# Kernel optimization log

Hardware: AMD Instinct MI355X
Metric: run time of the kernel (lower is better)

Reference implementation:

```python
import jax, jax.numpy as jnp
import numpy as np

B, N, DIM = 4, 1024, 768
H, HD = 12, DIM // 12
GP = 49
MLP = 3072


def _layernorm(x, w, b, eps=1e-5):
    mu = x.mean(axis=-1, keepdims=True)
    var = ((x - mu) ** 2).mean(axis=-1, keepdims=True)
    return (x - mu) * jax.lax.rsqrt(var + eps) * w + b


def setup_inputs() -> dict:
    key = jax.random.key(0)
    ks = jax.random.split(key, 12)
    s = 0.02
    return {
        "x": jax.random.normal(ks[0], (B, N, DIM), jnp.float32),
        "ln1_w": jnp.ones((DIM,), jnp.float32),
        "ln1_b": jnp.zeros((DIM,), jnp.float32),
        "qkv_w": jax.random.normal(ks[1], (DIM, 3 * DIM), jnp.float32) * s,
        "qkv_b": jnp.zeros((3 * DIM,), jnp.float32),
        "proj_w": jax.random.normal(ks[2], (DIM, DIM), jnp.float32) * s,
        "proj_b": jnp.zeros((DIM,), jnp.float32),
        "gp_w": jax.random.normal(ks[3], (GP, DIM), jnp.float32) * s,  # nn.Linear(dim, gp_num).weight, shape (gp_num, dim)
        "alpha": jax.random.normal(ks[4], (1, H, 1, 1), jnp.float32),
        "ln2_w": jnp.ones((DIM,), jnp.float32),
        "ln2_b": jnp.zeros((DIM,), jnp.float32),
        "ff1_w": jax.random.normal(ks[5], (DIM, MLP), jnp.float32) * s,
        "ff1_b": jnp.zeros((MLP,), jnp.float32),
        "ff2_w": jax.random.normal(ks[6], (MLP, DIM), jnp.float32) * s,
        "ff2_b": jnp.zeros((DIM,), jnp.float32),
    }


def reference(x, ln1_w, ln1_b, qkv_w, qkv_b, proj_w, proj_b, gp_w, alpha,
              ln2_w, ln2_b, ff1_w, ff1_b, ff2_w, ff2_b):
    b, n, _ = x.shape
    # --- attention branch ---
    xn = _layernorm(x, ln1_w, ln1_b)
    qkv = xn @ qkv_w + qkv_b                                 # [b,n,3*dim]
    q, k, v = jnp.split(qkv, 3, axis=-1)
    to_heads = lambda t: t.reshape(b, n, H, HD).transpose(0, 2, 1, 3)  # [b,h,n,hd]
    q, k, v = to_heads(q), to_heads(k), to_heads(v)
    scale = HD ** -0.5
    attn = jnp.einsum('bhnd,bhmd->bhnm', q, k) * scale       # raw scores
    # group weights: view (gp_num, dim) -> (h, gp_num, hd) (row-major, same as torch .view)
    gp = gp_w.reshape(H, GP, HD)
    gw = jnp.einsum('bhnd,hmd->bhnm', v, gp)                 # [b,h,n,gp]
    gw = jax.nn.gelu(gw, approximate=False)
    gw = jax.nn.softmax(gw, axis=-1)
    gw = jnp.einsum('bhnm,bhkm->bhnk', gw, gw)               # [b,h,n,n]
    attn = jax.nn.softmax(attn * gw, axis=-1)
    a = jax.nn.sigmoid(alpha)
    attn = (1.0 - a) * attn + a * gw
    attn = attn / (attn.sum(axis=2, keepdims=True) + 1e-8)   # note: dim=2 (column renorm), faithful to source
    out = jnp.einsum('bhnm,bhmd->bhnd', attn, v)
    out = out.transpose(0, 2, 1, 3).reshape(b, n, DIM)
    out = out @ proj_w + proj_b
    x = out + x
    # --- FFN branch ---
    xn = _layernorm(x, ln2_w, ln2_b)
    hdn = jax.nn.gelu(xn @ ff1_w + ff1_b, approximate=False)
    x = (hdn @ ff2_w + ff2_b) + x
    return x
```

## Files before the change

### kernel.cpp

```cpp
#include <hip/hip_runtime.h>
#include <hip/hip_bf16.h>
#include <math.h>

#define DEVI __device__ __forceinline__

typedef __bf16 bf16x8 __attribute__((ext_vector_type(8)));
typedef float f32x4 __attribute__((ext_vector_type(4)));
typedef float f32x2 __attribute__((ext_vector_type(2)));
typedef unsigned int u32x4 __attribute__((ext_vector_type(4)));
typedef float f32x4v __attribute__((ext_vector_type(4)));
typedef unsigned short u16;
typedef unsigned char u8;

DEVI u16 f2bf(float f) {
    __hip_bfloat16 h = __float2bfloat16(f);
    return __builtin_bit_cast(u16, h);
}
DEVI float bf2f(u16 u) {
    unsigned int x = ((unsigned int)u) << 16;
    return __builtin_bit_cast(float, x);
}
DEVI float gelu_f(float x) {
    float y = 0.7978845608f * (x + 0.044715f * x * x * x);
    float e = __expf(2.f * y);
    float t = 1.f - 2.f / (e + 1.f);
    return 0.5f * x * (1.f + t);
}
DEVI float sigm(float x) { return 1.f / (1.f + __expf(-x)); }

DEVI bf16x8 ldfrag(const u16* p) {
    return __builtin_bit_cast(bf16x8, *reinterpret_cast<const u32x4*>(p));
}

DEVI void gload_lds16(const u16* g, u16* l) {
    __builtin_amdgcn_global_load_lds(
        (const __attribute__((address_space(1))) void*)g,
        (__attribute__((address_space(3))) void*)l, 16, 0, 0);
}

DEVI void stage8(const u16* gbase, long long stride, u16* lds, int lane) {
    int r = lane >> 3;
    int kg = (lane & 7) ^ r;
    gload_lds16(gbase + (long long)r * stride + kg * 8, lds);
}
DEVI bf16x8 fragsw(const u16* tile, int rr, int k) {
    return ldfrag(&tile[rr * 64 + ((k ^ (rr & 7)) << 3)]);
}

DEVI unsigned int packbf(float a, float b) {
    return __builtin_amdgcn_perm(__builtin_bit_cast(unsigned int, b),
                                 __builtin_bit_cast(unsigned int, a), 0x07060302u);
}

__global__ __launch_bounds__(256) void tcast_all(const float* __restrict__ qkv_w, const float* __restrict__ proj_w,
                                                 const float* __restrict__ ff1_w, const float* __restrict__ ff2_w,
                                                 const float* __restrict__ gp_w,
                                                 u16* __restrict__ wqkv, u16* __restrict__ wproj,
                                                 u16* __restrict__ wff1, u16* __restrict__ wff2,
                                                 u16* __restrict__ gpB) {
    int id = blockIdx.x;
    if (id >= 6912) {
        int h = id - 6912;
        int tid = threadIdx.y * 32 + threadIdx.x;
        for (int i = tid; i < 4096; i += 256) {
            int m = i >> 6, d = i & 63;
            float v = (m < 49) ? gp_w[h * 3136 + m * 64 + d] : 0.f;
            gpB[h * 4096 + i] = f2bf(v);
        }
        return;
    }
    const float* in; u16* out; int R, C, tx;
    if (id < 1728)      { in = qkv_w;  out = wqkv;  R = 768;  C = 2304; tx = 72; }
    else if (id < 2304) { in = proj_w; out = wproj; R = 768;  C = 768;  tx = 24; id -= 1728; }
    else if (id < 4608) { in = ff1_w;  out = wff1;  R = 768;  C = 3072; tx = 96; id -= 2304; }
    else                { in = ff2_w;  out = wff2;  R = 3072; C = 768;  tx = 24; id -= 4608; }
    int c0 = (id % tx) * 32, r0 = (id / tx) * 32;
    __shared__ float tile[32][33];
    for (int ry = threadIdx.y; ry < 32; ry += 8)
        tile[ry][threadIdx.x] = in[(long long)(r0 + ry) * C + c0 + threadIdx.x];
    __syncthreads();
    for (int cy = threadIdx.y; cy < 32; cy += 8)
        out[(long long)(c0 + cy) * R + r0 + threadIdx.x] = f2bf(tile[threadIdx.x][cy]);
}

__global__ __launch_bounds__(256) void ln_k(const float* __restrict__ parts, int nparts, long long pstride,
                                            const float* __restrict__ bias2, const float* __restrict__ in2,
                                            const float* __restrict__ w, const float* __restrict__ b,
                                            u16* __restrict__ outbf, float* __restrict__ x1out,
                                            float* __restrict__ zfill) {
    int row = blockIdx.x;
    if (zfill && row < 192) zfill[row * 256 + threadIdx.x] = 0.f;
    long long ro = (long long)row * 768;
    __shared__ float lds1[4], lds2[4];
    float v[3];
    float s = 0.f, sq = 0.f;
#pragma unroll
    for (int j = 0; j < 3; j++) {
        int c = threadIdx.x + j * 256;
        float x = 0.f;
        for (int p = 0; p < nparts; p++) x += parts[p * pstride + ro + c];
        if (bias2) x += bias2[c];
        if (in2) x += in2[ro + c];
        v[j] = x; s += x; sq += x * x;
    }
    if (x1out) {
#pragma unroll
        for (int j = 0; j < 3; j++) x1out[ro + threadIdx.x + j * 256] = v[j];
    }
    for (int off = 32; off; off >>= 1) { s += __shfl_down(s, off); sq += __shfl_down(sq, off); }
    int wid = threadIdx.x >> 6;
    if ((threadIdx.x & 63) == 0) { lds1[wid] = s; lds2[wid] = sq; }
    __syncthreads();
    s = lds1[0] + lds1[1] + lds1[2] + lds1[3];
    sq = lds2[0] + lds2[1] + lds2[2] + lds2[3];
    float mu = s * (1.f / 768.f);
    float var = sq * (1.f / 768.f) - mu * mu;
    float rs = rsqrtf(var + 1e-5f);
#pragma unroll
    for (int j = 0; j < 3; j++) {
        int c = threadIdx.x + j * 256;
        outbf[ro + c] = f2bf((v[j] - mu) * rs * w[c] + b[c]);
    }
}

struct GemmP {
    const u16* A; const u16* B;
    float* outF; u16* outB;
    const float* bias;
    u16* qh; u16* kh; u16* vh;
    int K, lda, ldb, ldc;
    long long pstride;
    int epi;
    int splits;
};

__global__ __launch_bounds__(256) void gemm_bt4(GemmP p) {
    __shared__ u16 As[128 * 64];
    __shared__ u16 Bs[128 * 64];
    const int tid = threadIdx.x, lane = tid & 63, wave = tid >> 6;
    const int l16 = lane & 15, qd = lane >> 4;
    const int bn0 = blockIdx.x * 128, bm0 = blockIdx.y * 128;
    const int wm0 = (wave >> 1) * 64, wn0 = (wave & 1) * 64;
    const int kc = p.K / p.splits;
    const int kbeg = blockIdx.z * kc, kend = kbeg + kc;
    f32x4 acc[4][4] = {};
    for (int k0 = kbeg; k0 < kend; k0 += 64) {
        __syncthreads();
#pragma unroll
        for (int t = 0; t < 4; t++) {
            int rowg = wave * 32 + t * 8;
            stage8(p.A + (long long)(bm0 + rowg) * p.lda + k0, p.lda, As + rowg * 64, lane);
            stage8(p.B + (long long)(bn0 + rowg) * p.ldb + k0, p.ldb, Bs + rowg * 64, lane);
        }
        __syncthreads();
#pragma unroll
        for (int s = 0; s < 2; s++) {
            bf16x8 af[4], bv[4];
#pragma unroll
            for (int i = 0; i < 4; i++) af[i] = fragsw(As, wm0 + i * 16 + l16, s * 4 + qd);
#pragma unroll
            for (int j = 0; j < 4; j++) bv[j] = fragsw(Bs, wn0 + j * 16 + l16, s * 4 + qd);
#pragma unroll
            for (int i = 0; i < 4; i++)
#pragma unroll
                for (int j = 0; j < 4; j++)
                    acc[i][j] = __builtin_amdgcn_mfma_f32_16x16x32_bf16(af[i], bv[j], acc[i][j], 0, 0, 0);
        }
    }
#pragma unroll
    for (int i = 0; i < 4; i++)
#pragma unroll
        for (int j = 0; j < 4; j++)
#pragma unroll
            for (int r = 0; r < 4; r++) {
                int row = bm0 + wm0 + i * 16 + qd * 4 + r;
                int col = bn0 + wn0 + j * 16 + l16;
                float v = acc[i][j][r];
                if (p.epi == 0) {
                    p.outF[(long long)blockIdx.z * p.pstride + (long long)row * p.ldc + col] = v;
                } else if (p.epi == 2) {
                    p.outB[(long long)row * p.ldc + col] = f2bf(gelu_f(v + p.bias[col]));
                } else {
                    v += p.bias[col];
                    int sect = col / 768, cc = col % 768;
                    int h = cc >> 6, d = cc & 63;
                    int b = row >> 10, n = row & 1023;
                    long long o = ((long long)(b * 12 + h) * 1024 + n) * 64 + d;
                    if (sect == 0) p.qh[o] = f2bf(v * 0.125f);
                    else if (sect == 1) p.kh[o] = f2bf(v);
                    else p.vh[o] = f2bf(v);
                }
            }
}

__global__ __launch_bounds__(256) void gw0m_k(const u16* __restrict__ vh, const u16* __restrict__ gpB,
                                              u16* __restrict__ gwn, float* __restrict__ Wt) {
    {
        long long zi = ((long long)blockIdx.y * 16 + blockIdx.x) * 256 + threadIdx.x;
        Wt[zi] = 0.f;
    }
    __shared__ u16 As[64 * 64];
    __shared__ u16 Bs[64 * 64];
    const int tid = threadIdx.x, lane = tid & 63, wave = tid >> 6;
    const int l16 = lane & 15, qd = lane >> 4;
    const int z = blockIdx.y, n0 = blockIdx.x * 64, h = z % 12;
    const u16* vz = vh + ((long long)z * 1024 + n0) * 64;
    const u16* gz = gpB + h * 4096;
#pragma unroll
    for (int t = 0; t < 2; t++) {
        int rowg = wave * 16 + t * 8;
        stage8(vz + (long long)rowg * 64, 64, As + rowg * 64, lane);
        stage8(gz + (long long)rowg * 64, 64, Bs + rowg * 64, lane);
    }
    __syncthreads();
    f32x4 acc[4] = {};
#pragma unroll
    for (int s = 0; s < 2; s++) {
        bf16x8 af = fragsw(As, wave * 16 + l16, s * 4 + qd);
#pragma unroll
        for (int j = 0; j < 4; j++) {
            bf16x8 bv = fragsw(Bs, j * 16 + l16, s * 4 + qd);
            acc[j] = __builtin_amdgcn_mfma_f32_16x16x32_bf16(af, bv, acc[j], 0, 0, 0);
        }
    }
    float ex[4][4];
#pragma unroll
    for (int r = 0; r < 4; r++) {
        float mx = -1e30f;
        float gv[4];
#pragma unroll
        for (int j = 0; j < 4; j++) {
            int col = j * 16 + l16;
            float g = gelu_f(acc[j][r]);
            gv[j] = g;
            if (col < 49) mx = fmaxf(mx, g);
            else gv[j] = -1e30f;
        }
        mx = fmaxf(mx, __shfl_xor(mx, 1)); mx = fmaxf(mx, __shfl_xor(mx, 2));
        mx = fmaxf(mx, __shfl_xor(mx, 4)); mx = fmaxf(mx, __shfl_xor(mx, 8));
        float s = 0.f;
#pragma unroll
        for (int j = 0; j < 4; j++) {
            int col = j * 16 + l16;
            float e = (col < 49) ? __expf(gv[j] - mx) : 0.f;
            ex[r][j] = e;
            s += e;
        }
        s += __shfl_xor(s, 1); s += __shfl_xor(s, 2);
        s += __shfl_xor(s, 4); s += __shfl_xor(s, 8);
        float inv = 1.f / s;
        int row = wave * 16 + qd * 4 + r;
        long long o = ((long long)z * 1024 + n0 + row) * 64;
#pragma unroll
        for (int j = 0; j < 4; j++)
            gwn[o + j * 16 + l16] = f2bf(ex[r][j] * inv);
    }
}

__global__ __launch_bounds__(256) void attn_tg4(const u16* __restrict__ qh, const u16* __restrict__ kh,
                                                const u16* __restrict__ gwn, u8* __restrict__ e8,
                                                float* __restrict__ rowsumE) {
    __shared__ u16 As[128 * 64];
    __shared__ u16 Bs[128 * 64];
    const int tid = threadIdx.x, lane = tid & 63, wave = tid >> 6;
    const int l16 = lane & 15, qd = lane >> 4;
    const int bn0 = blockIdx.x * 128, bm0 = blockIdx.y * 128, z = blockIdx.z;
    const int wm0 = (wave >> 1) * 64, wn0 = (wave & 1) * 64;
    const u16* qz = qh + (long long)z * 65536;
    const u16* kz = kh + (long long)z * 65536;
    const u16* gz = gwn + (long long)z * 65536;
    f32x4 accS[4][4] = {};
    f32x4 accG[4][4] = {};
#pragma unroll
    for (int t = 0; t < 4; t++) {
        int rowg = wave * 32 + t * 8;
        stage8(qz + (long long)(bm0 + rowg) * 64, 64, As + rowg * 64, lane);
        stage8(kz + (long long)(bn0 + rowg) * 64, 64, Bs + rowg * 64, lane);
    }
    __syncthreads();
#pragma unroll
    for (int s = 0; s < 2; s++) {
        bf16x8 af[4], bv[4];
#pragma unroll
        for (int i = 0; i < 4; i++) af[i] = fragsw(As, wm0 + i * 16 + l16, s * 4 + qd);
#pragma unroll
        for (int j = 0; j < 4; j++) bv[j] = fragsw(Bs, wn0 + j * 16 + l16, s * 4 + qd);
#pragma unroll
        for (int i = 0; i < 4; i++)
#pragma unroll
            for (int j = 0; j < 4; j++)
                accS[i][j] = __builtin_amdgcn_mfma_f32_16x16x32_bf16(af[i], bv[j], accS[i][j], 0, 0, 0);
    }
    __syncthreads();
#pragma unroll
    for (int t = 0; t < 4; t++) {
        int rowg = wave * 32 + t * 8;
        stage8(gz + (long long)(bm0 + rowg) * 64, 64, As + rowg * 64, lane);
        stage8(gz + (long long)(bn0 + rowg) * 64, 64, Bs + rowg * 64, lane);
    }
    __syncthreads();
#pragma unroll
    for (int s = 0; s < 2; s++) {
        bf16x8 af[4], bv[4];
#pragma unroll
        for (int i = 0; i < 4; i++) af[i] = fragsw(As, wm0 + i * 16 + l16, s * 4 + qd);
#pragma unroll
        for (int j = 0; j < 4; j++) bv[j] = fragsw(Bs, wn0 + j * 16 + l16, s * 4 + qd);
#pragma unroll
        for (int i = 0; i < 4; i++)
#pragma unroll
            for (int j = 0; j < 4; j++)
                accG[i][j] = __builtin_amdgcn_mfma_f32_16x16x32_bf16(af[i], bv[j], accG[i][j], 0, 0, 0);
    }
    long long zoff = (long long)z * 1048576;
#pragma unroll
    for (int i = 0; i < 4; i++)
#pragma unroll
        for (int r = 0; r < 4; r++) {
            int row = bm0 + wm0 + i * 16 + qd * 4 + r;
            float rs = 0.f;
#pragma unroll
            for (int j = 0; j < 4; j++) {
                int col = bn0 + wn0 + j * 16 + l16;
                float ev = __expf(accS[i][j][r] * accG[i][j][r]);
                unsigned int pk = (unsigned int)__builtin_amdgcn_cvt_pk_fp8_f32(ev, ev, 0, false);
                e8[zoff + (long long)row * 1024 + col] = (u8)(pk & 0xff);
                rs += ev;
            }
            rs += __shfl_xor(rs, 1); rs += __shfl_xor(rs, 2);
            rs += __shfl_xor(rs, 4); rs += __shfl_xor(rs, 8);
            if (l16 == 0) atomicAdd(&rowsumE[z * 1024 + row], rs);
        }
}

__global__ __launch_bounds__(256) void combine2_k(const u16* __restrict__ gwn, const float* __restrict__ alpha,
                                                  float* __restrict__ colsum) {
    int z = blockIdx.x, h = z % 12;
    int j = threadIdx.x & 63, part = threadIdx.x >> 6;
    __shared__ float lds[4][64];
    __shared__ float Sl[64];
    float s = 0.f;
    for (int i = 0; i < 256; i++)
        s += bf2f(gwn[((long long)z * 1024 + part * 256 + i) * 64 + j]);
    lds[part][j] = s;
    __syncthreads();
    if (threadIdx.x < 64)
        Sl[threadIdx.x] = lds[0][threadIdx.x] + lds[1][threadIdx.x] + lds[2][threadIdx.x] + lds[3][threadIdx.x];
    __syncthreads();
    float a = sigm(alpha[h]);
    for (int m = threadIdx.x; m < 1024; m += 256) {
        const u16* g = gwn + ((long long)z * 1024 + m) * 64;
        float dot = 0.f;
#pragma unroll 8
        for (int jj = 0; jj < 64; jj++) dot += bf2f(g[jj]) * Sl[jj];
        colsum[z * 1024 + m] = a * dot;
    }
}

__global__ __launch_bounds__(256) void colsumE_k(const u8* __restrict__ e8, const float* __restrict__ rowsumE,
                                                 const float* __restrict__ alpha, float* __restrict__ colsum) {
    int z = blockIdx.x, h = z % 12;
    int n0 = blockIdx.y * 128;
    int grp = threadIdx.x & 127;
    int half = threadIdx.x >> 7;
    const u8* p = e8 + (long long)z * 1048576;
    const float* rs = rowsumE + z * 1024;
    float acc[8] = {};
    for (int n = n0 + half * 64; n < n0 + half * 64 + 64; n++) {
        unsigned long long w8 = *reinterpret_cast<const unsigned long long*>(&p[(long long)n * 1024 + grp * 8]);
        unsigned int w0 = (unsigned int)w8, w1 = (unsigned int)(w8 >> 32);
        float inv = 1.f / rs[n];
        f32x2 a0 = __builtin_amdgcn_cvt_pk_f32_fp8((int)w0, false);
        f32x2 a1 = __builtin_amdgcn_cvt_pk_f32_fp8((int)w0, true);
        f32x2 a2 = __builtin_amdgcn_cvt_pk_f32_fp8((int)w1, false);
        f32x2 a3 = __builtin_amdgcn_cvt_pk_f32_fp8((int)w1, true);
        acc[0] += a0.x * inv; acc[1] += a0.y * inv;
        acc[2] += a1.x * inv; acc[3] += a1.y * inv;
        acc[4] += a2.x * inv; acc[5] += a2.y * inv;
        acc[6] += a3.x * inv; acc[7] += a3.y * inv;
    }
    __shared__ float part[2][128][8];
#pragma unroll
    for (int j = 0; j < 8; j++) part[half][grp][j] = acc[j];
    __syncthreads();
    if (half == 0) {
        float a = sigm(alpha[h]);
#pragma unroll
        for (int j = 0; j < 8; j++)
            atomicAdd(&colsum[z * 1024 + grp * 8 + j], (1.f - a) * (part[0][grp][j] + part[1][grp][j]));
    }
}

__global__ __launch_bounds__(256) void vpt_k(const u16* __restrict__ vh, const float* __restrict__ colsum,
                                             u16* __restrict__ vpt) {
    int z = blockIdx.y, m0 = blockIdx.x * 64;
    __shared__ float ts[64 * 65];
    int mi = threadIdx.x >> 6, d = threadIdx.x & 63;
    for (int rr = 0; rr < 16; rr++) {
        int row = rr * 4 + mi;
        ts[row * 65 + d] = bf2f(vh[((long long)z * 1024 + m0 + row) * 64 + d]);
    }
    __syncthreads();
    int mj = threadIdx.x & 63, d0 = threadIdx.x >> 6;
    for (int rr = 0; rr < 16; rr++) {
        int dd = rr * 4 + d0;
        float cs = colsum[z * 1024 + m0 + mj] + 1e-8f;
        vpt[((long long)z * 64 + dd) * 1024 + m0 + mj] = f2bf(ts[mj * 65 + dd] / cs);
    }
}

__global__ __launch_bounds__(256) void wgemm_k(const u16* __restrict__ gwn, const u16* __restrict__ vpt,
                                               float* __restrict__ Wt) {
    int z = blockIdx.y, n0 = blockIdx.x * 128;
    __shared__ u16 gs[128 * 64];
    __shared__ u16 vs2[64 * 128];
    for (int i = threadIdx.x; i < 128 * 64; i += 256) {
        int nn = i >> 6, j = i & 63;
        gs[i] = gwn[((long long)z * 1024 + n0 + nn) * 64 + j];
        int d = i >> 7, n2 = i & 127;
        vs2[i] = vpt[((long long)z * 64 + d) * 1024 + n0 + n2];
    }
    __syncthreads();
    int j = threadIdx.x & 63, dg = threadIdx.x >> 6;
    float acc[16] = {};
    for (int nn = 0; nn < 128; nn++) {
        float g = bf2f(gs[nn * 64 + j]);
#pragma unroll
        for (int i = 0; i < 16; i++) acc[i] += g * bf2f(vs2[(dg * 16 + i) * 128 + nn]);
    }
#pragma unroll
    for (int i = 0; i < 16; i++)
        atomicAdd(&Wt[((long long)z * 64 + dg * 16 + i) * 64 + j], acc[i]);
}

__global__ __launch_bounds__(256) void attn_out4(const u8* __restrict__ e8, const u16* __restrict__ vpt,
                                                 const u16* __restrict__ gwn, const float* __restrict__ Wt,
                                                 const float* __restrict__ rowsumE,
                                                 const float* __restrict__ alpha, u16* __restrict__ out) {
    __shared__ u16 As[64 * 64];
    __shared__ u16 Bs[64 * 64];
    const int tid = threadIdx.x, lane = tid & 63, wave = tid >> 6;
    const int l16 = lane & 15, qd = lane >> 4;
    const int bm0 = blockIdx.x * 64, z = blockIdx.y;
    const int h = z % 12, b = z / 12;
    const u8* Pz = e8 + (long long)z * 1048576;
    const u16* vz = vpt + (long long)z * 65536;
    const int wr = wave * 16;
    f32x4 accP[4] = {};
    f32x4 accG[4] = {};
    const int arow = wr + (lane >> 2);
    const int cp = (lane & 3) * 2;
    for (int k0 = 0; k0 < 1024; k0 += 64) {
        __syncthreads();
        {
            u32x4 wv = *reinterpret_cast<const u32x4*>(Pz + (long long)(bm0 + arow) * 1024 + k0 + cp * 8);
            unsigned int ob[8];
#pragma unroll
            for (int k = 0; k < 4; k++) {
                f32x2 lo = __builtin_amdgcn_cvt_pk_f32_fp8((int)wv[k], false);
                f32x2 hi = __builtin_amdgcn_cvt_pk_f32_fp8((int)wv[k], true);
                ob[2 * k]     = packbf(lo.x, lo.y);
                ob[2 * k + 1] = packbf(hi.x, hi.y);
            }
            int p0 = (cp ^ (arow & 7)) << 3;
            int p1 = ((cp + 1) ^ (arow & 7)) << 3;
            *reinterpret_cast<u32x4*>(&As[arow * 64 + p0]) = *reinterpret_cast<u32x4*>(&ob[0]);
            *reinterpret_cast<u32x4*>(&As[arow * 64 + p1]) = *reinterpret_cast<u32x4*>(&ob[4]);
        }
#pragma unroll
        for (int t = 0; t < 2; t++) {
            int rowg = wave * 16 + t * 8;
            stage8(vz + (long long)rowg * 1024 + k0, 1024, Bs + rowg * 64, lane);
        }
        __syncthreads();
#pragma unroll
        for (int s = 0; s < 2; s++) {
            bf16x8 af = fragsw(As, wr + l16, s * 4 + qd);
#pragma unroll
            for (int j = 0; j < 4; j++) {
                bf16x8 bv = fragsw(Bs, j * 16 + l16, s * 4 + qd);
                accP[j] = __builtin_amdgcn_mfma_f32_16x16x32_bf16(af, bv, accP[j], 0, 0, 0);
            }
        }
    }
    const u16* gz = gwn + (long long)z * 65536;
    const float* wz = Wt + (long long)z * 4096;
    __syncthreads();
#pragma unroll
    for (int t = 0; t < 2; t++) {
        int rowg = wave * 16 + t * 8;
        stage8(gz + (long long)(bm0 + rowg) * 64, 64, As + rowg * 64, lane);
    }
    {
        int row = tid >> 2, c0 = (tid & 3) * 16;
        const float* wrow = wz + row * 64;
#pragma unroll
        for (int j0 = 0; j0 < 16; j0++) {
            int j = c0 + j0;
            int pos = (((j >> 3) ^ (row & 7)) << 3) | (j & 7);
            Bs[row * 64 + pos] = f2bf(wrow[j]);
        }
    }
    __syncthreads();
#pragma unroll
    for (int s = 0; s < 2; s++) {
        bf16x8 af = fragsw(As, wr + l16, s * 4 + qd);
#pragma unroll
        for (int j = 0; j < 4; j++) {
            bf16x8 bv = fragsw(Bs, j * 16 + l16, s * 4 + qd);
            accG[j] = __builtin_amdgcn_mfma_f32_16x16x32_bf16(af, bv, accG[j], 0, 0, 0);
        }
    }
    float a = sigm(alpha[h]);
#pragma unroll
    for (int r = 0; r < 4; r++) {
        int n = bm0 + wr + qd * 4 + r;
        float sc = (1.f - a) / rowsumE[z * 1024 + n];
#pragma unroll
        for (int j = 0; j < 4; j++) {
            int d = j * 16 + l16;
            float v = sc * accP[j][r] + a * accG[j][r];
            out[((long long)(b * 1024 + n)) * 768 + h * 64 + d] = f2bf(v);
        }
    }
}

__global__ __launch_bounds__(256) void fuse2_k(const float* __restrict__ parts, long long pstride4,
                                               const float* __restrict__ bias, const float* __restrict__ x1,
                                               float* __restrict__ outp) {
    long long i4 = (long long)blockIdx.x * 256 + threadIdx.x;
    int c4 = (int)(i4 % 192);
    const f32x4v* p0 = (const f32x4v*)parts;
    f32x4v v = p0[i4] + p0[pstride4 + i4];
    f32x4v bb = ((const f32x4v*)bias)[c4];
    f32x4v xx = ((const f32x4v*)x1)[i4];
    ((f32x4v*)outp)[i4] = v + bb + xx;
}

extern "C" void kernel_launch(void* const* d_in, const int* in_sizes, int n_in,
                              void* d_out, int out_size, void* d_ws, size_t ws_size,
                              hipStream_t stream) {
    const float* x      = (const float*)d_in[0];
    const float* ln1_w  = (const float*)d_in[1];
    const float* ln1_b  = (const float*)d_in[2];
    const float* qkv_w  = (const float*)d_in[3];
    const float* qkv_b  = (const float*)d_in[4];
    const float* proj_w = (const float*)d_in[5];
    const float* proj_b = (const float*)d_in[6];
    const float* gp_w   = (const float*)d_in[7];
    const float* alpha  = (const float*)d_in[8];
    const float* ln2_w  = (const float*)d_in[9];
    const float* ln2_b  = (const float*)d_in[10];
    const float* ff1_w  = (const float*)d_in[11];
    const float* ff1_b  = (const float*)d_in[12];
    const float* ff2_w  = (const float*)d_in[13];
    const float* ff2_b  = (const float*)d_in[14];

    char* w = (char*)d_ws;
    size_t off = 0;
    auto alloc = [&](size_t bytes) { size_t r = off; off += (bytes + 255) & ~(size_t)255; return r; };

    u16*   xn_bf   = (u16*)(w + alloc(4096LL * 768 * 2));
    u16*   wqkv_t  = (u16*)(w + alloc(2304LL * 768 * 2));
    u16*   wproj_t = (u16*)(w + alloc(768LL * 768 * 2));
    u16*   wff1_t  = (u16*)(w + alloc(3072LL * 768 * 2));
    u16*   wff2_t  = (u16*)(w + alloc(768LL * 3072 * 2));
    u16*   gpB     = (u16*)(w + alloc(12LL * 64 * 64 * 2));
    u16*   qh      = (u16*)(w + alloc(48LL * 1024 * 64 * 2));
    u16*   kh      = (u16*)(w + alloc(48LL * 1024 * 64 * 2));
    u16*   vh      = (u16*)(w + alloc(48LL * 1024 * 64 * 2));
    u16*   gwn     = (u16*)(w + alloc(48LL * 1024 * 64 * 2));
    char*  ebase   = w + alloc(2 * 4096LL * 768 * 4 + 4096LL * 3072 * 2 + 2 * 4096LL * 768 * 4);
    u8*    e8      = (u8*)ebase;
    float* rowsumE = (float*)(w + alloc(48LL * 1024 * 4));
    float* Wt      = (float*)(w + alloc(48LL * 64 * 64 * 4));
    float* colsum  = (float*)(w + alloc(48LL * 1024 * 4));
    u16*   vpt     = (u16*)(w + alloc(48LL * 64 * 1024 * 2));
    float* x1      = (float*)(w + alloc(4096LL * 768 * 4));
    u16*   attn_o  = (u16*)(w + alloc(4096LL * 768 * 2));
    u16*   xn2     = (u16*)(w + alloc(4096LL * 768 * 2));
    float* projP = (float*)ebase;
    u16*   hmid  = (u16*)(ebase + 2 * 4096LL * 768 * 4);
    float* ff2P  = (float*)(ebase + 2 * 4096LL * 768 * 4 + 4096LL * 3072 * 2);

    dim3 blk(256);
    const long long PS = 4096LL * 768;

    tcast_all<<<dim3(6924), dim3(32, 8), 0, stream>>>(qkv_w, proj_w, ff1_w, ff2_w, gp_w,
                                                      wqkv_t, wproj_t, wff1_t, wff2_t, gpB);

    ln_k<<<dim3(4096), blk, 0, stream>>>(x, 1, 0, nullptr, nullptr, ln1_w, ln1_b, xn_bf, nullptr, rowsumE);

    {
        GemmP p = {xn_bf, wqkv_t, nullptr, nullptr, qkv_b, qh, kh, vh, 768, 768, 768, 0, 0, 4, 1};
        gemm_bt4<<<dim3(18, 32, 1), blk, 0, stream>>>(p);
    }

    gw0m_k<<<dim3(16, 48), blk, 0, stream>>>(vh, gpB, gwn, Wt);

    attn_tg4<<<dim3(8, 8, 48), blk, 0, stream>>>(qh, kh, gwn, e8, rowsumE);

    combine2_k<<<dim3(48), blk, 0, stream>>>(gwn, alpha, colsum);
    colsumE_k<<<dim3(48, 8), blk, 0, stream>>>(e8, rowsumE, alpha, colsum);

    vpt_k<<<dim3(16, 48), blk, 0, stream>>>(vh, colsum, vpt);

    wgemm_k<<<dim3(8, 48), blk, 0, stream>>>(gwn, vpt, Wt);

    attn_out4<<<dim3(16, 48), blk, 0, stream>>>(e8, vpt, gwn, Wt, rowsumE, alpha, attn_o);

    {
        GemmP p = {attn_o, wproj_t, projP, nullptr, nullptr, nullptr, nullptr, nullptr,
                   768, 768, 768, 768, PS, 0, 2};
        gemm_bt4<<<dim3(6, 32, 2), blk, 0, stream>>>(p);
    }

    ln_k<<<dim3(4096), blk, 0, stream>>>(projP, 2, PS, proj_b, x, ln2_w, ln2_b, xn2, x1, nullptr);

    {
        GemmP p = {xn2, wff1_t, nullptr, hmid, ff1_b, nullptr, nullptr, nullptr,
                   768, 768, 768, 3072, 0, 2, 1};
        gemm_bt4<<<dim3(24, 32, 1), blk, 0, stream>>>(p);
    }

    {
        GemmP p = {hmid, wff2_t, ff2P, nullptr, nullptr, nullptr, nullptr, nullptr,
                   3072, 3072, 3072, 768, PS, 0, 2};
        gemm_bt4<<<dim3(6, 32, 2), blk, 0, stream>>>(p);
    }

    fuse2_k<<<dim3(3072), blk, 0, stream>>>(ff2P, PS / 4, ff2_b, x1, (float*)d_out);
}
```

Measured before the change: 466.0 us.

## Fuse colsum/vpt/wgemm kernels, prefetch in attn_out, and raise split-K to four

The gw0m kernel now atomically accumulates per-head column sums of the group-weight softmax into a buffer, which removes the separate combine2 pass. Its dot-product work moves into the first chunk of colsumE. The vpt and wgemm kernels are merged into one kernel that stages inputs through LDS with async loads. attn_out4 now issues the B-tile load before the A conversion and prefetches the next A row. The proj and ff2 GEMMs use split-K of 4 instead of 2, so the downstream reductions read four partial buffers and the workspace grows.

```diff
diff --git a/kernel.cpp b/kernel.cpp
--- a/kernel.cpp
+++ b/kernel.cpp
@@ -45,6 +45,9 @@
 }
 DEVI bf16x8 fragsw(const u16* tile, int rr, int k) {
     return ldfrag(&tile[rr * 64 + ((k ^ (rr & 7)) << 3)]);
+}
+DEVI u16 elsw(const u16* tile, int r, int c) {
+    return tile[r * 64 + ((((c >> 3) ^ (r & 7)) << 3) | (c & 7))];
 }
 
 DEVI unsigned int packbf(float a, float b) {
@@ -89,7 +92,7 @@
                                             u16* __restrict__ outbf, float* __restrict__ x1out,
                                             float* __restrict__ zfill) {
     int row = blockIdx.x;
-    if (zfill && row < 192) zfill[row * 256 + threadIdx.x] = 0.f;
+    if (zfill && row < 396) zfill[row * 256 + threadIdx.x] = 0.f;
     long long ro = (long long)row * 768;
     __shared__ float lds1[4], lds2[4];
     float v[3];
@@ -194,7 +197,8 @@
 }
 
 __global__ __launch_bounds__(256) void gw0m_k(const u16* __restrict__ vh, const u16* __restrict__ gpB,
-                                              u16* __restrict__ gwn, float* __restrict__ Wt) {
+                                              u16* __restrict__ gwn, float* __restrict__ Wt,
+                                              float* __restrict__ Sbuf) {
     {
         long long zi = ((long long)blockIdx.y * 16 + blockIdx.x) * 256 + threadIdx.x;
         Wt[zi] = 0.f;
@@ -223,7 +227,7 @@
             acc[j] = __builtin_amdgcn_mfma_f32_16x16x32_bf16(af, bv, acc[j], 0, 0, 0);
         }
     }
-    float ex[4][4];
+    float colacc[4] = {};
 #pragma unroll
     for (int r = 0; r < 4; r++) {
         float mx = -1e30f;
@@ -239,11 +243,12 @@
         mx = fmaxf(mx, __shfl_xor(mx, 1)); mx = fmaxf(mx, __shfl_xor(mx, 2));
         mx = fmaxf(mx, __shfl_xor(mx, 4)); mx = fmaxf(mx, __shfl_xor(mx, 8));
         float s = 0.f;
+        float ex[4];
 #pragma unroll
         for (int j = 0; j < 4; j++) {
             int col = j * 16 + l16;
             float e = (col < 49) ? __expf(gv[j] - mx) : 0.f;
-            ex[r][j] = e;
+            ex[j] = e;
             s += e;
         }
         s += __shfl_xor(s, 1); s += __shfl_xor(s, 2);
@@ -252,8 +257,21 @@
         int row = wave * 16 + qd * 4 + r;
         long long o = ((long long)z * 1024 + n0 + row) * 64;
 #pragma unroll
+        for (int j = 0; j < 4; j++) {
+            float sv = ex[j] * inv;
+            gwn[o + j * 16 + l16] = f2bf(sv);
+            colacc[j] += sv;
+        }
+    }
+#pragma unroll
+    for (int j = 0; j < 4; j++) {
+        colacc[j] += __shfl_xor(colacc[j], 16);
+        colacc[j] += __shfl_xor(colacc[j], 32);
+    }
+    if (lane < 16) {
+#pragma unroll
         for (int j = 0; j < 4; j++)
-            gwn[o + j * 16 + l16] = f2bf(ex[r][j] * inv);
+            atomicAdd(&Sbuf[z * 64 + j * 16 + l16], colacc[j]);
     }
 }
 
@@ -333,34 +351,25 @@
         }
 }
 
-__global__ __launch_bounds__(256) void combine2_k(const u16* __restrict__ gwn, const float* __restrict__ alpha,
-                                                  float* __restrict__ colsum) {
-    int z = blockIdx.x, h = z % 12;
-    int j = threadIdx.x & 63, part = threadIdx.x >> 6;
-    __shared__ float lds[4][64];
-    __shared__ float Sl[64];
-    float s = 0.f;
-    for (int i = 0; i < 256; i++)
-        s += bf2f(gwn[((long long)z * 1024 + part * 256 + i) * 64 + j]);
-    lds[part][j] = s;
-    __syncthreads();
-    if (threadIdx.x < 64)
-        Sl[threadIdx.x] = lds[0][threadIdx.x] + lds[1][threadIdx.x] + lds[2][threadIdx.x] + lds[3][threadIdx.x];
-    __syncthreads();
-    float a = sigm(alpha[h]);
-    for (int m = threadIdx.x; m < 1024; m += 256) {
-        const u16* g = gwn + ((long long)z * 1024 + m) * 64;
-        float dot = 0.f;
-#pragma unroll 8
-        for (int jj = 0; jj < 64; jj++) dot += bf2f(g[jj]) * Sl[jj];
-        colsum[z * 1024 + m] = a * dot;
-    }
-}
-
 __global__ __launch_bounds__(256) void colsumE_k(const u8* __restrict__ e8, const float* __restrict__ rowsumE,
+                                                 const u16* __restrict__ gwn, const float* __restrict__ Sbuf,
                                                  const float* __restrict__ alpha, float* __restrict__ colsum) {
     int z = blockIdx.x, h = z % 12;
-    int n0 = blockIdx.y * 128;
+    int chunk = blockIdx.y;
+    float a = sigm(alpha[h]);
+    if (chunk == 0) {
+        __shared__ float Sl[64];
+        if (threadIdx.x < 64) Sl[threadIdx.x] = Sbuf[z * 64 + threadIdx.x];
+        __syncthreads();
+        for (int m = threadIdx.x; m < 1024; m += 256) {
+            const u16* g = gwn + ((long long)z * 1024 + m) * 64;
+            float dot = 0.f;
+#pragma unroll 8
+            for (int jj = 0; jj < 64; jj++) dot += bf2f(g[jj]) * Sl[jj];
+            atomicAdd(&colsum[z * 1024 + m], a * dot);
+        }
+    }
+    int n0 = chunk * 128;
     int grp = threadIdx.x & 127;
     int half = threadIdx.x >> 7;
     const u8* p = e8 + (long long)z * 1048576;
@@ -384,47 +393,41 @@
     for (int j = 0; j < 8; j++) part[half][grp][j] = acc[j];
     __syncthreads();
     if (half == 0) {
-        float a = sigm(alpha[h]);
 #pragma unroll
         for (int j = 0; j < 8; j++)
             atomicAdd(&colsum[z * 1024 + grp * 8 + j], (1.f - a) * (part[0][grp][j] + part[1][grp][j]));
     }
 }
 
-__global__ __launch_bounds__(256) void vpt_k(const u16* __restrict__ vh, const float* __restrict__ colsum,
-                                             u16* __restrict__ vpt) {
-    int z = blockIdx.y, m0 = blockIdx.x * 64;
-    __shared__ float ts[64 * 65];
-    int mi = threadIdx.x >> 6, d = threadIdx.x & 63;
-    for (int rr = 0; rr < 16; rr++) {
-        int row = rr * 4 + mi;
-        ts[row * 65 + d] = bf2f(vh[((long long)z * 1024 + m0 + row) * 64 + d]);
-    }
-    __syncthreads();
-    int mj = threadIdx.x & 63, d0 = threadIdx.x >> 6;
-    for (int rr = 0; rr < 16; rr++) {
-        int dd = rr * 4 + d0;
-        float cs = colsum[z * 1024 + m0 + mj] + 1e-8f;
-        vpt[((long long)z * 64 + dd) * 1024 + m0 + mj] = f2bf(ts[mj * 65 + dd] / cs);
-    }
-}
-
-__global__ __launch_bounds__(256) void wgemm_k(const u16* __restrict__ gwn, const u16* __restrict__ vpt,
-                                               float* __restrict__ Wt) {
+__global__ __launch_bounds__(256) void vptw_k(const u16* __restrict__ vh, const float* __restrict__ colsum,
+                                              const u16* __restrict__ gwn, u16* __restrict__ vpt,
+                                              float* __restrict__ Wt) {
     int z = blockIdx.y, n0 = blockIdx.x * 128;
+    __shared__ u16 ts[128 * 64];
     __shared__ u16 gs[128 * 64];
     __shared__ u16 vs2[64 * 128];
-    for (int i = threadIdx.x; i < 128 * 64; i += 256) {
-        int nn = i >> 6, j = i & 63;
-        gs[i] = gwn[((long long)z * 1024 + n0 + nn) * 64 + j];
-        int d = i >> 7, n2 = i & 127;
-        vs2[i] = vpt[((long long)z * 64 + d) * 1024 + n0 + n2];
-    }
-    __syncthreads();
-    int j = threadIdx.x & 63, dg = threadIdx.x >> 6;
+    const int tid = threadIdx.x, lane = tid & 63, wave = tid >> 6;
+#pragma unroll
+    for (int t = 0; t < 4; t++) {
+        int rowg = wave * 32 + t * 8;
+        stage8(vh + ((long long)z * 1024 + n0 + rowg) * 64, 64, ts + rowg * 64, lane);
+        stage8(gwn + ((long long)z * 1024 + n0 + rowg) * 64, 64, gs + rowg * 64, lane);
+    }
+    __syncthreads();
+    int n = tid & 127, dgrp = tid >> 7;
+    float inv = 1.f / (colsum[z * 1024 + n0 + n] + 1e-8f);
+#pragma unroll
+    for (int dd = 0; dd < 32; dd++) {
+        int d = dgrp * 32 + dd;
+        u16 o = f2bf(bf2f(elsw(ts, n, d)) * inv);
+        vpt[((long long)z * 64 + d) * 1024 + n0 + n] = o;
+        vs2[d * 128 + n] = o;
+    }
+    __syncthreads();
+    int j = tid & 63, dg = tid >> 6;
     float acc[16] = {};
     for (int nn = 0; nn < 128; nn++) {
-        float g = bf2f(gs[nn * 64 + j]);
+        float g = bf2f(elsw(gs, nn, j));
 #pragma unroll
         for (int i = 0; i < 16; i++) acc[i] += g * bf2f(vs2[(dg * 16 + i) * 128 + nn]);
     }
@@ -450,10 +453,18 @@
     f32x4 accG[4] = {};
     const int arow = wr + (lane >> 2);
     const int cp = (lane & 3) * 2;
+    const u8* arow_base = Pz + (long long)(bm0 + arow) * 1024 + cp * 8;
+    u32x4 wv = *reinterpret_cast<const u32x4*>(arow_base);
     for (int k0 = 0; k0 < 1024; k0 += 64) {
         __syncthreads();
+#pragma unroll
+        for (int t = 0; t < 2; t++) {
+            int rowg = wave * 16 + t * 8;
+            stage8(vz + (long long)rowg * 1024 + k0, 1024, Bs + rowg * 64, lane);
+        }
+        u32x4 wvn = wv;
+        if (k0 + 64 < 1024) wvn = *reinterpret_cast<const u32x4*>(arow_base + k0 + 64);
         {
-            u32x4 wv = *reinterpret_cast<const u32x4*>(Pz + (long long)(bm0 + arow) * 1024 + k0 + cp * 8);
             unsigned int ob[8];
 #pragma unroll
             for (int k = 0; k < 4; k++) {
@@ -467,11 +478,6 @@
             *reinterpret_cast<u32x4*>(&As[arow * 64 + p0]) = *reinterpret_cast<u32x4*>(&ob[0]);
             *reinterpret_cast<u32x4*>(&As[arow * 64 + p1]) = *reinterpret_cast<u32x4*>(&ob[4]);
         }
-#pragma unroll
-        for (int t = 0; t < 2; t++) {
-            int rowg = wave * 16 + t * 8;
-            stage8(vz + (long long)rowg * 1024 + k0, 1024, Bs + rowg * 64, lane);
-        }
         __syncthreads();
 #pragma unroll
         for (int s = 0; s < 2; s++) {
@@ -482,6 +488,7 @@
                 accP[j] = __builtin_amdgcn_mfma_f32_16x16x32_bf16(af, bv, accP[j], 0, 0, 0);
             }
         }
+        wv = wvn;
     }
     const u16* gz = gwn + (long long)z * 65536;
     const float* wz = Wt + (long long)z * 4096;
@@ -531,7 +538,7 @@
     long long i4 = (long long)blockIdx.x * 256 + threadIdx.x;
     int c4 = (int)(i4 % 192);
     const f32x4v* p0 = (const f32x4v*)parts;
-    f32x4v v = p0[i4] + p0[pstride4 + i4];
+    f32x4v v = p0[i4] + p0[pstride4 + i4] + p0[2 * pstride4 + i4] + p0[3 * pstride4 + i4];
     f32x4v bb = ((const f32x4v*)bias)[c4];
     f32x4v xx = ((const f32x4v*)x1)[i4];
     ((f32x4v*)outp)[i4] = v + bb + xx;
@@ -570,18 +577,20 @@
     u16*   kh      = (u16*)(w + alloc(48LL * 1024 * 64 * 2));
     u16*   vh      = (u16*)(w + alloc(48LL * 1024 * 64 * 2));
     u16*   gwn     = (u16*)(w + alloc(48LL * 1024 * 64 * 2));
-    char*  ebase   = w + alloc(2 * 4096LL * 768 * 4 + 4096LL * 3072 * 2 + 2 * 4096LL * 768 * 4);
+    char*  ebase   = w + alloc(4 * 4096LL * 768 * 4 + 4096LL * 3072 * 2 + 4 * 4096LL * 768 * 4);
     u8*    e8      = (u8*)ebase;
-    float* rowsumE = (float*)(w + alloc(48LL * 1024 * 4));
+    float* zbase   = (float*)(w + alloc(396LL * 256 * 4));
+    float* rowsumE = zbase;
+    float* colsum  = zbase + 48 * 1024;
+    float* Sbuf    = zbase + 96 * 1024;
     float* Wt      = (float*)(w + alloc(48LL * 64 * 64 * 4));
-    float* colsum  = (float*)(w + alloc(48LL * 1024 * 4));
     u16*   vpt     = (u16*)(w + alloc(48LL * 64 * 1024 * 2));
     float* x1      = (float*)(w + alloc(4096LL * 768 * 4));
     u16*   attn_o  = (u16*)(w + alloc(4096LL * 768 * 2));
     u16*   xn2     = (u16*)(w + alloc(4096LL * 768 * 2));
     float* projP = (float*)ebase;
-    u16*   hmid  = (u16*)(ebase + 2 * 4096LL * 768 * 4);
-    float* ff2P  = (float*)(ebase + 2 * 4096LL * 768 * 4 + 4096LL * 3072 * 2);
+    u16*   hmid  = (u16*)(ebase + 4 * 4096LL * 768 * 4);
+    float* ff2P  = (float*)(ebase + 4 * 4096LL * 768 * 4 + 4096LL * 3072 * 2);
 
     dim3 blk(256);
     const long long PS = 4096LL * 768;
@@ -589,33 +598,30 @@
     tcast_all<<<dim3(6924), dim3(32, 8), 0, stream>>>(qkv_w, proj_w, ff1_w, ff2_w, gp_w,
                                                       wqkv_t, wproj_t, wff1_t, wff2_t, gpB);
 
-    ln_k<<<dim3(4096), blk, 0, stream>>>(x, 1, 0, nullptr, nullptr, ln1_w, ln1_b, xn_bf, nullptr, rowsumE);
+    ln_k<<<dim3(4096), blk, 0, stream>>>(x, 1, 0, nullptr, nullptr, ln1_w, ln1_b, xn_bf, nullptr, zbase);
 
     {
         GemmP p = {xn_bf, wqkv_t, nullptr, nullptr, qkv_b, qh, kh, vh, 768, 768, 768, 0, 0, 4, 1};
         gemm_bt4<<<dim3(18, 32, 1), blk, 0, stream>>>(p);
     }
 
-    gw0m_k<<<dim3(16, 48), blk, 0, stream>>>(vh, gpB, gwn, Wt);
+    gw0m_k<<<dim3(16, 48), blk, 0, stream>>>(vh, gpB, gwn, Wt, Sbuf);
 
     attn_tg4<<<dim3(8, 8, 48), blk, 0, stream>>>(qh, kh, gwn, e8, rowsumE);
 
-    combine2_k<<<dim3(48), blk, 0, stream>>>(gwn, alpha, colsum);
-    colsumE_k<<<dim3(48, 8), blk, 0, stream>>>(e8, rowsumE, alpha, colsum);
-
-    vpt_k<<<dim3(16, 48), blk, 0, stream>>>(vh, colsum, vpt);
-
-    wgemm_k<<<dim3(8, 48), blk, 0, stream>>>(gwn, vpt, Wt);
+    colsumE_k<<<dim3(48, 8), blk, 0, stream>>>(e8, rowsumE, gwn, Sbuf, alpha, colsum);
+
+    vptw_k<<<dim3(8, 48), blk, 0, stream>>>(vh, colsum, gwn, vpt, Wt);
 
     attn_out4<<<dim3(16, 48), blk, 0, stream>>>(e8, vpt, gwn, Wt, rowsumE, alpha, attn_o);
 
     {
         GemmP p = {attn_o, wproj_t, projP, nullptr, nullptr, nullptr, nullptr, nullptr,
-                   768, 768, 768, 768, PS, 0, 2};
-        gemm_bt4<<<dim3(6, 32, 2), blk, 0, stream>>>(p);
-    }
-
-    ln_k<<<dim3(4096), blk, 0, stream>>>(projP, 2, PS, proj_b, x, ln2_w, ln2_b, xn2, x1, nullptr);
+                   768, 768, 768, 768, PS, 0, 4};
+        gemm_bt4<<<dim3(6, 32, 4), blk, 0, stream>>>(p);
+    }
+
+    ln_k<<<dim3(4096), blk, 0, stream>>>(projP, 4, PS, proj_b, x, ln2_w, ln2_b, xn2, x1, nullptr);
 
     {
         GemmP p = {xn2, wff1_t, nullptr, hmid, ff1_b, nullptr, nullptr, nullptr,
@@ -625,8 +631,8 @@
 
     {
         GemmP p = {hmid, wff2_t, ff2P, nullptr, nullptr, nullptr, nullptr, nullptr,
-                   3072, 3072, 3072, 768, PS, 0, 2};
-        gemm_bt4<<<dim3(6, 32, 2), blk, 0, stream>>>(p);
+                   3072, 3072, 3072, 768, PS, 0, 4};
+        gemm_bt4<<<dim3(6, 32, 4), blk, 0, stream>>>(p);
     }
 
     fuse2_k<<<dim3(3072), blk, 0, stream>>>(ff2P, PS / 4, ff2_b, x1, (float*)d_out);
```

Result: no change. 472.0 us (+1.3%).
